# Kernel tuning notes

Hardware: AMD Instinct MI355X
Metric: run time of the kernel (lower is better)

Reference implementation:

```python
import jax, jax.numpy as jnp
import numpy as np

SEQ_LEN, BATCH = 1024, 256
VOCAB, EMBED, HIDDEN = 32000, 512, 1024


def setup_inputs() -> dict:
    key = jax.random.key(0)
    k1, k2, k3, k4, k5, k6 = jax.random.split(key, 6)
    return {
        "x_seq": jax.random.randint(k1, (SEQ_LEN, BATCH), 0, VOCAB, dtype=jnp.int64)
        if jax.config.jax_enable_x64 else jax.random.randint(k1, (SEQ_LEN, BATCH), 0, VOCAB, dtype=jnp.int32),
        "emb": jax.random.normal(k2, (VOCAB, EMBED), dtype=jnp.float32) * 0.02,
        "W_ih": jax.random.normal(k3, (HIDDEN, EMBED), dtype=jnp.float32) * 0.02,
        "b_ih": jax.random.normal(k4, (HIDDEN,), dtype=jnp.float32) * 0.02,
        "W_hh": jax.random.normal(k5, (HIDDEN, HIDDEN), dtype=jnp.float32) * 0.02,
        "b_hh": jax.random.normal(k6, (HIDDEN,), dtype=jnp.float32) * 0.02,
    }


def reference(x_seq, emb, W_ih, b_ih, W_hh, b_hh):
    # x_seq: [S, B] int -> embedded: [S, B, E]
    embedded = emb[x_seq]
    # Input projection is time-independent: batch it into one big GEMM
    # (same math as per-step W_ih(x_t) + bias in the torch loop).
    x_proj = jnp.einsum("sbe,he->sbh", embedded, W_ih) + b_ih  # [S, B, H]

    h0 = jnp.zeros((x_seq.shape[1], W_hh.shape[0]), dtype=emb.dtype)

    def step(h, xp_t):
        # h_{t} = tanh(W_ih x_t + b_ih + W_hh h_{t-1} + b_hh)
        h_new = jnp.tanh(xp_t + h @ W_hh.T + b_hh)
        return h_new, h_new

    _, hidden_states = jax.lax.scan(step, h0, x_proj)  # [S, B, H]
    return hidden_states
```

## Files before the change

kernel.cpp:

```cpp
#include <hip/hip_runtime.h>
#include <hip/hip_bf16.h>

typedef unsigned short u16;
typedef unsigned int u32;
typedef unsigned long long u64;
typedef __attribute__((ext_vector_type(8))) short short8v;
typedef __attribute__((ext_vector_type(8))) unsigned short ushort8v;
typedef __attribute__((ext_vector_type(4))) float float4v;
typedef __attribute__((ext_vector_type(4))) unsigned int uint4v;

#define S_LEN 1024
#define BATCH 256
#define VOCAB 32000
#define EMBED 512
#define HIDDEN 1024
#define BH (BATCH * HIDDEN)
#define FLAG_STRIDE 32

__device__ inline u16 f2bf(float f) {
  return __builtin_bit_cast(u16, __float2bfloat16(f));
}

__device__ inline short8v cohload16(const u16* base, int voff) {
  __amdgpu_buffer_rsrc_t r =
      __builtin_amdgcn_make_buffer_rsrc((void*)base, (short)0, -1, 0x00020000);
  uint4v d = __builtin_amdgcn_raw_buffer_load_b128(r, voff, 0, 17);
  return __builtin_bit_cast(short8v, d);
}
__device__ inline void cohstore16(u16* base, int voff, ushort8v v) {
  __amdgpu_buffer_rsrc_t r =
      __builtin_amdgcn_make_buffer_rsrc((void*)base, (short)0, -1, 0x00020000);
  __builtin_amdgcn_raw_buffer_store_b128(__builtin_bit_cast(uint4v, v), r, voff, 0, 17);
}

__device__ inline short8v cvt8(float4v a, float4v b) {
  ushort8v v;
  v[0]=f2bf(a[0]); v[1]=f2bf(a[1]); v[2]=f2bf(a[2]); v[3]=f2bf(a[3]);
  v[4]=f2bf(b[0]); v[5]=f2bf(b[1]); v[6]=f2bf(b[2]); v[7]=f2bf(b[3]);
  return __builtin_bit_cast(short8v, v);
}

__global__ __launch_bounds__(256) void prep_kernel(u16* __restrict__ ws16) {
  int i = blockIdx.x * 256 + threadIdx.x;
  ushort8v z = {0,0,0,0,0,0,0,0};
  *(ushort8v*)(ws16 + (size_t)i * 8) = z;
}

__global__ __launch_bounds__(256, 1) void rnn_fused(const int* __restrict__ xseq,
                                                    const float* __restrict__ emb,
                                                    const float* __restrict__ wih,
                                                    const float* __restrict__ bih,
                                                    const float* __restrict__ whh,
                                                    const float* __restrict__ bhh,
                                                    u16* __restrict__ hbuf,
                                                    float* __restrict__ out,
                                                    u32* __restrict__ flag) {
  __shared__ float red[4][16][68];
  __shared__ u16 xq[S_LEN * 16];
  const int tid = threadIdx.x;
  const int lane = tid & 63, w = tid >> 6;
  const int l15 = lane & 15, l4 = lane >> 4;
  const int g = blockIdx.x & 15;
  const int jt = blockIdx.x >> 4;

  short8v Wf[4][8];
  #pragma unroll
  for (int jj = 0; jj < 4; jj++)
    #pragma unroll
    for (int kq = 0; kq < 8; kq++) {
      const float* s = whh + (size_t)(jt * 64 + jj * 16 + l15) * HIDDEN
                       + w * 256 + kq * 32 + l4 * 8;
      Wf[jj][kq] = cvt8(*(const float4v*)s, *(const float4v*)(s + 4));
    }
  short8v Wihf[4][4];
  #pragma unroll
  for (int jj = 0; jj < 4; jj++)
    #pragma unroll
    for (int kk = 0; kk < 4; kk++) {
      const float* s = wih + (size_t)(jt * 64 + jj * 16 + l15) * EMBED
                       + w * 128 + kk * 32 + l4 * 8;
      Wihf[jj][kk] = cvt8(*(const float4v*)s, *(const float4v*)(s + 4));
    }
  for (int i = tid; i < S_LEN * 16; i += 256)
    xq[i] = (u16)xseq[(i >> 4) * BATCH + g * 16 + (i & 15)];
  const int trow = w * 4 + (lane >> 3);
  const int tc0 = (lane & 7) * 8;
  float bsum[8];
  #pragma unroll
  for (int i = 0; i < 8; i++)
    bsum[i] = bhh[jt * 64 + tc0 + i] + bih[jt * 64 + tc0 + i];
  const int aoff = ((g * 16 + l15) * HIDDEN + w * 256 + l4 * 8) * 2;
  __syncthreads();

  float4v xacc[4] = {};
  {
    const float* er = emb + (size_t)xq[l15] * EMBED + w * 128 + l4 * 8;
    #pragma unroll
    for (int kk = 0; kk < 4; kk++) {
      short8v af = cvt8(*(const float4v*)(er + kk * 32),
                        *(const float4v*)(er + kk * 32 + 4));
      #pragma unroll
      for (int jj = 0; jj < 4; jj++)
        xacc[jj] = __builtin_amdgcn_mfma_f32_16x16x32_bf16(af, Wihf[jj][kk], xacc[jj], 0, 0, 0);
    }
  }

  for (int t = 0; t < S_LEN; t++) {
    const int p = t & 1;
    float* outt = out + (size_t)t * BH;
    float4v accp[4] = {xacc[0], xacc[1], xacc[2], xacc[3]};
    int tn = (t + 1 < S_LEN) ? (t + 1) : t;
    const float* er = emb + (size_t)xq[tn * 16 + l15] * EMBED + w * 128 + l4 * 8;
    float4v e[8];
    #pragma unroll
    for (int kk = 0; kk < 4; kk++) {
      e[2 * kk]     = *(const float4v*)(er + kk * 32);
      e[2 * kk + 1] = *(const float4v*)(er + kk * 32 + 4);
    }
    if (t > 0) {
      if (lane < 16) {
        const u32* f = flag + ((size_t)(g * 16 + w * 4 + (lane >> 2)) * 4 + (lane & 3)) * FLAG_STRIDE;
        while (__hip_atomic_load(f, __ATOMIC_RELAXED, __HIP_MEMORY_SCOPE_AGENT) < (u32)t) { }
      }
    }
    __builtin_amdgcn_sched_barrier(0);
    const u16* hp = hbuf + (size_t)p * BH;
    short8v a[8];
    #pragma unroll
    for (int kq = 0; kq < 8; kq++)
      a[kq] = cohload16(hp, aoff + kq * 64);
    float4v xn[4] = {};
    #pragma unroll
    for (int kk = 0; kk < 4; kk++) {
      short8v af = cvt8(e[2 * kk], e[2 * kk + 1]);
      #pragma unroll
      for (int jj = 0; jj < 4; jj++)
        xn[jj] = __builtin_amdgcn_mfma_f32_16x16x32_bf16(af, Wihf[jj][kk], xn[jj], 0, 0, 0);
    }
    #pragma unroll
    for (int kq = 0; kq < 8; kq++)
      #pragma unroll
      for (int jj = 0; jj < 4; jj++)
        accp[jj] = __builtin_amdgcn_mfma_f32_16x16x32_bf16(a[kq], Wf[jj][kq], accp[jj], 0, 0, 0);
    xacc[0] = xn[0]; xacc[1] = xn[1]; xacc[2] = xn[2]; xacc[3] = xn[3];
    #pragma unroll
    for (int jj = 0; jj < 4; jj++)
      #pragma unroll
      for (int q = 0; q < 4; q++)
        red[w][l4 * 4 + q][jj * 16 + l15] = accp[jj][q];
    __syncthreads();
    float sum[8];
    if (lane < 32) {
      float4v r0 = *(const float4v*)&red[0][trow][tc0];
      float4v r1 = *(const float4v*)&red[0][trow][tc0 + 4];
      float4v s0 = *(const float4v*)&red[1][trow][tc0];
      float4v s1 = *(const float4v*)&red[1][trow][tc0 + 4];
      float4v u0 = *(const float4v*)&red[2][trow][tc0];
      float4v u1 = *(const float4v*)&red[2][trow][tc0 + 4];
      float4v v0 = *(const float4v*)&red[3][trow][tc0];
      float4v v1 = *(const float4v*)&red[3][trow][tc0 + 4];
      #pragma unroll
      for (int i = 0; i < 4; i++) {
        sum[i]     = r0[i] + s0[i] + u0[i] + v0[i] + bsum[i];
        sum[i + 4] = r1[i] + s1[i] + u1[i] + v1[i] + bsum[i + 4];
      }
    }
    __syncthreads();
    if (lane < 32) {
      float th[8];
      #pragma unroll
      for (int i = 0; i < 8; i++) {
        float ex = __expf(-2.0f * fabsf(sum[i]));
        float v = (1.0f - ex) / (1.0f + ex);
        th[i] = copysignf(v, sum[i]);
      }
      float4v o0 = {th[0], th[1], th[2], th[3]};
      float4v o1 = {th[4], th[5], th[6], th[7]};
      float* op = outt + (size_t)(g * 16 + trow) * HIDDEN + jt * 64 + tc0;
      *(float4v*)op = o0;
      *(float4v*)(op + 4) = o1;
      ushort8v hv;
      #pragma unroll
      for (int i = 0; i < 8; i++) hv[i] = f2bf(th[i]);
      u16* hq = hbuf + (size_t)(p ^ 1) * BH;
      cohstore16(hq, ((g * 16 + trow) * HIDDEN + jt * 64 + tc0) * 2, hv);
    }
    asm volatile("s_waitcnt vmcnt(0)" ::: "memory");
    if (lane == 0)
      __hip_atomic_store(flag + ((size_t)(g * 16 + jt) * 4 + w) * FLAG_STRIDE,
                         (u32)(t + 1), __ATOMIC_RELAXED, __HIP_MEMORY_SCOPE_AGENT);
  }
}

extern "C" void kernel_launch(void* const* d_in, const int* in_sizes, int n_in,
                              void* d_out, int out_size, void* d_ws, size_t ws_size,
                              hipStream_t stream) {
  const int* xseq   = (const int*)d_in[0];
  const float* emb  = (const float*)d_in[1];
  const float* wih  = (const float*)d_in[2];
  const float* bih  = (const float*)d_in[3];
  const float* whh  = (const float*)d_in[4];
  const float* bhh  = (const float*)d_in[5];
  float* out = (float*)d_out;
  char* ws = (char*)d_ws;
  u16* hbuf = (u16*)ws;
  u32* flag = (u32*)(ws + 1048576);

  prep_kernel<<<288, 256, 0, stream>>>((u16*)ws);
  rnn_fused<<<256, 256, 0, stream>>>(xseq, emb, wih, bih, whh, bhh, hbuf, out, flag);
}
```

Baseline: 3.975 ms.

## Move next-step input projection off the recurrent critical path and widen epilogue lanes

Reorders the per-step schedule so the recurrent MFMAs, reduction, tanh, h store and flag publish happen before the next timestep's embedding loads and input-projection MFMAs. The next step's x-projection now overlaps other blocks' waiting rather than delaying the flag signal. The epilogue also spreads over all 64 lanes, each handling 4 outputs with a 64-bit coherent store instead of 32 lanes doing 8. The risk is that the embedding gather latency is less hidden, because it is issued after the h loads.

```diff
diff --git a/kernel.cpp b/kernel.cpp
--- a/kernel.cpp
+++ b/kernel.cpp
@@ -8,6 +8,7 @@
 typedef __attribute__((ext_vector_type(8))) unsigned short ushort8v;
 typedef __attribute__((ext_vector_type(4))) float float4v;
 typedef __attribute__((ext_vector_type(4))) unsigned int uint4v;
+typedef __attribute__((ext_vector_type(2))) unsigned int uint2v;
 
 #define S_LEN 1024
 #define BATCH 256
@@ -27,10 +28,10 @@
   uint4v d = __builtin_amdgcn_raw_buffer_load_b128(r, voff, 0, 17);
   return __builtin_bit_cast(short8v, d);
 }
-__device__ inline void cohstore16(u16* base, int voff, ushort8v v) {
+__device__ inline void cohstore8(u16* base, int voff, uint2v v) {
   __amdgpu_buffer_rsrc_t r =
       __builtin_amdgcn_make_buffer_rsrc((void*)base, (short)0, -1, 0x00020000);
-  __builtin_amdgcn_raw_buffer_store_b128(__builtin_bit_cast(uint4v, v), r, voff, 0, 17);
+  __builtin_amdgcn_raw_buffer_store_b64(v, r, voff, 0, 17);
 }
 
 __device__ inline short8v cvt8(float4v a, float4v b) {
@@ -83,13 +84,14 @@
     }
   for (int i = tid; i < S_LEN * 16; i += 256)
     xq[i] = (u16)xseq[(i >> 4) * BATCH + g * 16 + (i & 15)];
-  const int trow = w * 4 + (lane >> 3);
-  const int tc0 = (lane & 7) * 8;
-  float bsum[8];
+  const int trow = w * 4 + (lane >> 4);
+  const int tc4 = (lane & 15) * 4;
+  float bsum[4];
   #pragma unroll
-  for (int i = 0; i < 8; i++)
-    bsum[i] = bhh[jt * 64 + tc0 + i] + bih[jt * 64 + tc0 + i];
+  for (int i = 0; i < 4; i++)
+    bsum[i] = bhh[jt * 64 + tc4 + i] + bih[jt * 64 + tc4 + i];
   const int aoff = ((g * 16 + l15) * HIDDEN + w * 256 + l4 * 8) * 2;
+  const int hoff = ((g * 16 + trow) * HIDDEN + jt * 64 + tc4) * 2;
   __syncthreads();
 
   float4v xacc[4] = {};
@@ -109,14 +111,6 @@
     const int p = t & 1;
     float* outt = out + (size_t)t * BH;
     float4v accp[4] = {xacc[0], xacc[1], xacc[2], xacc[3]};
-    int tn = (t + 1 < S_LEN) ? (t + 1) : t;
-    const float* er = emb + (size_t)xq[tn * 16 + l15] * EMBED + w * 128 + l4 * 8;
-    float4v e[8];
-    #pragma unroll
-    for (int kk = 0; kk < 4; kk++) {
-      e[2 * kk]     = *(const float4v*)(er + kk * 32);
-      e[2 * kk + 1] = *(const float4v*)(er + kk * 32 + 4);
-    }
     if (t > 0) {
       if (lane < 16) {
         const u32* f = flag + ((size_t)(g * 16 + w * 4 + (lane >> 2)) * 4 + (lane & 3)) * FLAG_STRIDE;
@@ -129,6 +123,50 @@
     #pragma unroll
     for (int kq = 0; kq < 8; kq++)
       a[kq] = cohload16(hp, aoff + kq * 64);
+    __builtin_amdgcn_sched_barrier(0);
+    int tn = (t + 1 < S_LEN) ? (t + 1) : t;
+    const float* er = emb + (size_t)xq[tn * 16 + l15] * EMBED + w * 128 + l4 * 8;
+    float4v e[8];
+    #pragma unroll
+    for (int kk = 0; kk < 4; kk++) {
+      e[2 * kk]     = *(const float4v*)(er + kk * 32);
+      e[2 * kk + 1] = *(const float4v*)(er + kk * 32 + 4);
+    }
+    #pragma unroll
+    for (int kq = 0; kq < 8; kq++)
+      #pragma unroll
+      for (int jj = 0; jj < 4; jj++)
+        accp[jj] = __builtin_amdgcn_mfma_f32_16x16x32_bf16(a[kq], Wf[jj][kq], accp[jj], 0, 0, 0);
+    #pragma unroll
+    for (int jj = 0; jj < 4; jj++)
+      #pragma unroll
+      for (int q = 0; q < 4; q++)
+        red[w][l4 * 4 + q][jj * 16 + l15] = accp[jj][q];
+    __syncthreads();
+    float4v r0 = *(const float4v*)&red[0][trow][tc4];
+    float4v r1 = *(const float4v*)&red[1][trow][tc4];
+    float4v r2 = *(const float4v*)&red[2][trow][tc4];
+    float4v r3 = *(const float4v*)&red[3][trow][tc4];
+    __syncthreads();
+    float th[4];
+    #pragma unroll
+    for (int i = 0; i < 4; i++) {
+      float s = r0[i] + r1[i] + r2[i] + r3[i] + bsum[i];
+      float ex = __expf(-2.0f * fabsf(s));
+      float v = (1.0f - ex) / (1.0f + ex);
+      th[i] = copysignf(v, s);
+    }
+    float4v o = {th[0], th[1], th[2], th[3]};
+    *(float4v*)(outt + (size_t)(g * 16 + trow) * HIDDEN + jt * 64 + tc4) = o;
+    uint2v hv;
+    hv[0] = (u32)f2bf(th[0]) | ((u32)f2bf(th[1]) << 16);
+    hv[1] = (u32)f2bf(th[2]) | ((u32)f2bf(th[3]) << 16);
+    u16* hq = hbuf + (size_t)(p ^ 1) * BH;
+    cohstore8(hq, hoff, hv);
+    asm volatile("s_waitcnt vmcnt(0)" ::: "memory");
+    if (lane == 0)
+      __hip_atomic_store(flag + ((size_t)(g * 16 + jt) * 4 + w) * FLAG_STRIDE,
+                         (u32)(t + 1), __ATOMIC_RELAXED, __HIP_MEMORY_SCOPE_AGENT);
     float4v xn[4] = {};
     #pragma unroll
     for (int kk = 0; kk < 4; kk++) {
@@ -137,58 +175,7 @@
       for (int jj = 0; jj < 4; jj++)
         xn[jj] = __builtin_amdgcn_mfma_f32_16x16x32_bf16(af, Wihf[jj][kk], xn[jj], 0, 0, 0);
     }
-    #pragma unroll
-    for (int kq = 0; kq < 8; kq++)
-      #pragma unroll
-      for (int jj = 0; jj < 4; jj++)
-        accp[jj] = __builtin_amdgcn_mfma_f32_16x16x32_bf16(a[kq], Wf[jj][kq], accp[jj], 0, 0, 0);
     xacc[0] = xn[0]; xacc[1] = xn[1]; xacc[2] = xn[2]; xacc[3] = xn[3];
-    #pragma unroll
-    for (int jj = 0; jj < 4; jj++)
-      #pragma unroll
-      for (int q = 0; q < 4; q++)
-        red[w][l4 * 4 + q][jj * 16 + l15] = accp[jj][q];
-    __syncthreads();
-    float sum[8];
-    if (lane < 32) {
-      float4v r0 = *(const float4v*)&red[0][trow][tc0];
-      float4v r1 = *(const float4v*)&red[0][trow][tc0 + 4];
-      float4v s0 = *(const float4v*)&red[1][trow][tc0];
-      float4v s1 = *(const float4v*)&red[1][trow][tc0 + 4];
-      float4v u0 = *(const float4v*)&red[2][trow][tc0];
-      float4v u1 = *(const float4v*)&red[2][trow][tc0 + 4];
-      float4v v0 = *(const float4v*)&red[3][trow][tc0];
-      float4v v1 = *(const float4v*)&red[3][trow][tc0 + 4];
-      #pragma unroll
-      for (int i = 0; i < 4; i++) {
-        sum[i]     = r0[i] + s0[i] + u0[i] + v0[i] + bsum[i];
-        sum[i + 4] = r1[i] + s1[i] + u1[i] + v1[i] + bsum[i + 4];
-      }
-    }
-    __syncthreads();
-    if (lane < 32) {
-      float th[8];
-      #pragma unroll
-      for (int i = 0; i < 8; i++) {
-        float ex = __expf(-2.0f * fabsf(sum[i]));
-        float v = (1.0f - ex) / (1.0f + ex);
-        th[i] = copysignf(v, sum[i]);
-      }
-      float4v o0 = {th[0], th[1], th[2], th[3]};
-      float4v o1 = {th[4], th[5], th[6], th[7]};
-      float* op = outt + (size_t)(g * 16 + trow) * HIDDEN + jt * 64 + tc0;
-      *(float4v*)op = o0;
-      *(float4v*)(op + 4) = o1;
-      ushort8v hv;
-      #pragma unroll
-      for (int i = 0; i < 8; i++) hv[i] = f2bf(th[i]);
-      u16* hq = hbuf + (size_t)(p ^ 1) * BH;
-      cohstore16(hq, ((g * 16 + trow) * HIDDEN + jt * 64 + tc0) * 2, hv);
-    }
-    asm volatile("s_waitcnt vmcnt(0)" ::: "memory");
-    if (lane == 0)
-      __hip_atomic_store(flag + ((size_t)(g * 16 + jt) * 4 + w) * FLAG_STRIDE,
-                         (u32)(t + 1), __ATOMIC_RELAXED, __HIP_MEMORY_SCOPE_AGENT);
   }
 }
 
```

Result: faster. 3.342 ms (-15.9%).
